# Optimization experiments

Hardware: AMD Instinct MI355X
Metric: run time of the kernel (lower is better)

Reference implementation:

```python
import jax, jax.numpy as jnp
import numpy as np

NSAMPLE = 16   # knn neighbors for cost volume
KCLUST = 8     # cluster size stand-in for custom_cluster_pc1 (min_count=8)
B, N, D = 2, 4096, 64


def _sqdist(src, dst):
    # src [B,N,C], dst [B,M,C] -> [B,N,M]
    d = (jnp.sum(src * src, -1)[:, :, None]
         + jnp.sum(dst * dst, -1)[:, None, :]
         - 2.0 * jnp.einsum('bnc,bmc->bnm', src, dst))
    return jnp.maximum(d, 0.0)


def _knn(k, xyz, new_xyz):
    return jax.lax.top_k(-_sqdist(new_xyz, xyz), k)[1]  # [B,S,k] indices of k smallest


def _group(points, idx):
    # points [B,M,C], idx [B,N,K] -> [B,N,K,C]
    b = jnp.arange(points.shape[0])[:, None, None]
    return points[b, idx]


def _weightnet(x, w1, b1, w2, b2, w3, b3):
    # x [B,N,K,3]; 1x1 conv stack == per-point MLP, relu
    h = jax.nn.relu(jnp.einsum('bnkc,cd->bnkd', x, w1) + b1)
    h = jax.nn.relu(jnp.einsum('bnkc,cd->bnkd', h, w2) + b2)
    return jax.nn.relu(jnp.einsum('bnkc,cd->bnkd', h, w3) + b3)


def _leaky(x):
    return jnp.where(x > 0, x, 0.1 * x)


def _forward(xyz1, xyz2, points1, points2, vel1, vel2, mask1, mask2,
             w_xyz, w_vel, w_points,
             mlp_w1, mlp_b1, mlp_w2, mlp_b2,
             wn1_w1, wn1_b1, wn1_w2, wn1_b2, wn1_w3, wn1_b3,
             wn2_w1, wn2_b1, wn2_w2, wn2_b2, wn2_w3, wn2_b3):
    xyz1t = jnp.transpose(xyz1, (0, 2, 1))      # [B,N1,3]
    xyz2t = jnp.transpose(xyz2, (0, 2, 1))      # [B,N2,3]
    p1t = jnp.transpose(points1, (0, 2, 1))     # [B,N1,D1]
    p2t = jnp.transpose(points2, (0, 2, 1))     # [B,N2,D2]

    # --- custom_cluster_pc1 stand-in: knn clusters of pc1 with its velocities ---
    idx_c = _knn(KCLUST, xyz1t, xyz1t)                     # [B,N,KC]
    cc = _group(xyz1t, idx_c)                              # [B,N,KC,3]
    cv = _group(vel1[..., None], idx_c)[..., 0]            # [B,N,KC]

    u = cc / jnp.linalg.norm(cc, axis=-1, keepdims=True)
    ATA = jnp.einsum('bnki,bnkj->bnij', u, u) + 1e-6 * jnp.eye(3, dtype=u.dtype)
    ATb = jnp.einsum('bnki,bnk->bni', u, cv)
    v_world = jnp.linalg.solve(ATA, ATb[..., None])[..., 0]  # [B,N,3]

    # --- feature-space knn between weighted (xyz, points) concatenations ---
    f1 = jnp.concatenate([w_xyz * xyz1t, w_points * p1t], axis=-1)
    f2 = jnp.concatenate([w_xyz * xyz2t, w_points * p2t], axis=-1)
    knn_idx = _knn(NSAMPLE, f2, f1)                        # [B,N1,K]

    neighbor_xyz = _group(xyz2t, knn_idx)                  # [B,N1,K,3]
    direction_xyz = neighbor_xyz - xyz1t[:, :, None, :]
    g2 = _group(p2t, knn_idx)                              # [B,N1,K,D2]
    g1 = jnp.broadcast_to(p1t[:, :, None, :], g2.shape[:3] + (p1t.shape[-1],))
    new_points = jnp.concatenate([g1, g2, direction_xyz], axis=-1)  # [B,N1,K,D1+D2+3]

    h = _leaky(jnp.einsum('bnkc,cd->bnkd', new_points, mlp_w1) + mlp_b1)
    h = _leaky(jnp.einsum('bnkc,cd->bnkd', h, mlp_w2) + mlp_b2)    # [B,N1,K,128]

    w = _weightnet(direction_xyz, wn1_w1, wn1_b1, wn1_w2, wn1_b2, wn1_w3, wn1_b3)
    point_to_patch = jnp.sum(w * h, axis=2)                # [B,N1,128]

    # --- second grouping in rigid-velocity space ---
    idx2 = _knn(NSAMPLE, v_world, v_world)
    nxyz1 = _group(xyz1t, idx2)
    dir2 = nxyz1 - xyz1t[:, :, None, :]
    w2 = _weightnet(dir2, wn2_w1, wn2_b1, wn2_w2, wn2_b2, wn2_w3, wn2_b3)
    gcost = _group(point_to_patch, idx2)                   # [B,N1,K,128]
    patch_to_patch = jnp.sum(w2 * gcost, axis=2)           # [B,N1,128]

    return jnp.transpose(patch_to_patch, (0, 2, 1)), v_world  # [B,128,N1], [B,N1,3]


def setup_inputs() -> dict:
    key = jax.random.key(0)
    ks = jax.random.split(key, 24)
    s = 0.05
    inp = {
        'xyz1': jax.random.normal(ks[0], (B, 3, N), jnp.float32),
        'xyz2': jax.random.normal(ks[1], (B, 3, N), jnp.float32),
        'points1': jax.random.normal(ks[2], (B, D, N), jnp.float32),
        'points2': jax.random.normal(ks[3], (B, D, N), jnp.float32),
        'vel1': jax.random.normal(ks[4], (B, N), jnp.float32),
        'vel2': jax.random.normal(ks[5], (B, N), jnp.float32),
        'mask1': jnp.ones((B, N), jnp.float32),
        'mask2': jnp.ones((B, N), jnp.float32),
        'w_xyz': jnp.float32(0.4), 'w_vel': jnp.float32(0.2), 'w_points': jnp.float32(0.4),
        'mlp_w1': jax.random.normal(ks[6], (2 * D + 3, 128), jnp.float32) * s,
        'mlp_b1': jnp.zeros((128,), jnp.float32),
        'mlp_w2': jax.random.normal(ks[7], (128, 128), jnp.float32) * s,
        'mlp_b2': jnp.zeros((128,), jnp.float32),
    }
    for tag, base in (('wn1', 8), ('wn2', 14)):
        inp[f'{tag}_w1'] = jax.random.normal(ks[base], (3, 8), jnp.float32) * s
        inp[f'{tag}_b1'] = jnp.zeros((8,), jnp.float32)
        inp[f'{tag}_w2'] = jax.random.normal(ks[base + 1], (8, 8), jnp.float32) * s
        inp[f'{tag}_b2'] = jnp.zeros((8,), jnp.float32)
        inp[f'{tag}_w3'] = jax.random.normal(ks[base + 2], (8, 128), jnp.float32) * s
        inp[f'{tag}_b3'] = jnp.zeros((128,), jnp.float32)
    return inp


def reference(xyz1, xyz2, points1, points2, vel1, vel2, mask1, mask2,
              w_xyz, w_vel, w_points,
              mlp_w1, mlp_b1, mlp_w2, mlp_b2,
              wn1_w1, wn1_b1, wn1_w2, wn1_b2, wn1_w3, wn1_b3,
              wn2_w1, wn2_b1, wn2_w2, wn2_b2, wn2_w3, wn2_b3):
    return _forward(xyz1, xyz2, points1, points2, vel1, vel2, mask1, mask2,
                    w_xyz, w_vel, w_points,
                    mlp_w1, mlp_b1, mlp_w2, mlp_b2,
                    wn1_w1, wn1_b1, wn1_w2, wn1_b2, wn1_w3, wn1_b3,
                    wn2_w1, wn2_b1, wn2_w2, wn2_b2, wn2_w3, wn2_b3)
```

## Files before the change

### kernel.cpp

```cpp
#include <hip/hip_runtime.h>

#define NPTS 4096
#define NQ   8192
#define DD   64
#define KNN  16
#define KC   8
#define NSEG3 32
#define NPSEG 32
#define KB96 96
#define FSTR 104
#define VOFF 1048576

#define ALWAYS_INLINE __attribute__((always_inline)) inline

typedef __attribute__((ext_vector_type(8))) short bf16x8;
typedef __attribute__((ext_vector_type(4))) float f32x4;

__device__ ALWAYS_INLINE float leakyf(float x) { return x > 0.f ? x : 0.1f * x; }

__device__ ALWAYS_INLINE unsigned short bf16rne(float f) {
  unsigned u = __float_as_uint(f);
  u = (u + 0x7FFFu + ((u >> 16) & 1u)) >> 16;
  return (unsigned short)u;
}

__device__ ALWAYS_INLINE float packdt(float d, unsigned tag12) {
  return __uint_as_float((__float_as_uint(d) & 0xFFFFF000u) | tag12);
}

#define TK8_FOREACH(M)  M(0) M(1) M(2) M(3) M(4) M(5) M(6) M(7)
#define TK16_FOREACH(M) M(0) M(1) M(2) M(3) M(4) M(5) M(6) M(7) \
                        M(8) M(9) M(10) M(11) M(12) M(13) M(14) M(15)

#define TK_DECL1(i) float tkd##i = 3.4e38f; int tki##i = 0;
#define TK_STEP1(i) { bool c = vd < tkd##i; float t_ = tkd##i; int u_ = tki##i; \
                      tkd##i = c ? vd : tkd##i; tki##i = c ? vi : tki##i; \
                      vd = c ? t_ : vd; vi = c ? u_ : vi; }
#define TK8_DECL  TK8_FOREACH(TK_DECL1)
#define TK8_INS(dexp, mexp)  { float vd = (dexp); int vi = (mexp); \
                               if (vd < tkd7)  { TK8_FOREACH(TK_STEP1) } }
#define TK8_RESET1(i) tkd##i = 3.4e38f; tki##i = 0;

#define PK_DECL1(i) float pk##i = __uint_as_float(0x7F7FFFFFu);
#define PK_RESET1(i) pk##i = __uint_as_float(0x7F7FFFFFu);
#define PK_STEP1(i) { float lo_ = fminf(pk##i, pv); pv = fmaxf(pk##i, pv); pk##i = lo_; }
#define PK16_DECL    TK16_FOREACH(PK_DECL1)
#define PK16_INS(ve) { float pv = (ve); TK16_FOREACH(PK_STEP1) }
#define PK_STORE1(i) pdq[i] = pk##i;
#define PK16_STORE   TK16_FOREACH(PK_STORE1)

__global__ __launch_bounds__(256) void k_prep(
    const float* __restrict__ xyz1, const float* __restrict__ xyz2,
    const float* __restrict__ pts1, const float* __restrict__ pts2,
    const float* __restrict__ w_xyz_p, const float* __restrict__ w_points_p,
    unsigned short* __restrict__ f1b, unsigned short* __restrict__ f2b,
    float* __restrict__ n1, float* __restrict__ n2a,
    float* __restrict__ p1t, float* __restrict__ p2t,
    float* __restrict__ x1t, float* __restrict__ x2t)
{
  int tgid = blockIdx.x * 256 + threadIdx.x;
  int cloud = tgid >> 13;
  int gid = tgid & (NQ - 1);
  int b = gid >> 12, n = gid & (NPTS - 1);
  float wx = w_xyz_p[0], wp = w_points_p[0];
  const float* xyz = cloud ? xyz2 : xyz1;
  const float* pts = cloud ? pts2 : pts1;
  unsigned short* fb = cloud ? f2b : f1b;
  float* nrm = cloud ? n2a : n1;
  float* pt  = cloud ? p2t : p1t;
  float* xt  = cloud ? x2t : x1t;
  const float* xb = xyz + (size_t)b * 3 * NPTS;
  float x = xb[n], y = xb[NPTS + n], z = xb[2 * NPTS + n];
  float nrm2 = fmaf(z, z, fmaf(y, y, x * x));
  float4 xv; xv.x = x; xv.y = y; xv.z = z; xv.w = nrm2;
  *(float4*)&xt[(size_t)gid * 4] = xv;
  float fx = wx * x, fy = wx * y, fz = wx * z;
  float acc = fmaf(fz, fz, fmaf(fy, fy, fx * fx));
  unsigned short* fr = fb + (size_t)gid * KB96;
  fr[0] = bf16rne(fx); fr[1] = bf16rne(fy); fr[2] = bf16rne(fz);
  const float* pb = pts + (size_t)b * DD * NPTS;
  float* pr = pt + (size_t)gid * DD;
  for (int c = 0; c < DD; ++c) {
    float v = pb[(size_t)c * NPTS + n];
    pr[c] = v;
    float fv = wp * v;
    fr[3 + c] = bf16rne(fv);
    acc = fmaf(fv, fv, acc);
  }
  for (int c = 67; c < KB96; ++c) fr[c] = 0;
  nrm[gid] = acc;
}

__global__ __launch_bounds__(256) void k_knn3(
    const float* __restrict__ x4, float* __restrict__ pd, int* __restrict__ pi)
{
  __shared__ __align__(16) float4 sc[128];
  int seg = blockIdx.y;
  int Q = blockIdx.x * 256 + threadIdx.x;
  int b = Q >> 12;
  float4 q = *(const float4*)&x4[(size_t)Q * 4];
  TK8_DECL
  int gbase = (b << 12) + seg * 128;
  if (threadIdx.x < 128)
    sc[threadIdx.x] = *(const float4*)&x4[(size_t)(gbase + threadIdx.x) * 4];
  __syncthreads();
  int m0 = seg * 128;
#pragma unroll
  for (int j = 0; j < 128; ++j) {
    float4 c = sc[j];
    float dot = fmaf(q.z, c.z, fmaf(q.y, c.y, q.x * c.x));
    float d = fmaxf(q.w + c.w - 2.f * dot, 0.f);
    TK8_INS(d, m0 + j)
  }
  float* pdq = pd + ((size_t)Q * NSEG3 + seg) * 8;
  int* piq = pi + ((size_t)Q * NSEG3 + seg) * 8;
#define ST8(i) pdq[i] = tkd##i; piq[i] = tki##i;
  TK8_FOREACH(ST8)
#undef ST8
}

__global__ __launch_bounds__(256) void k_knnv(
    const float* __restrict__ x4, float* __restrict__ pd)
{
  __shared__ __align__(16) float4 sc[128];
  int seg = blockIdx.y;
  int Q = blockIdx.x * 256 + threadIdx.x;
  int b = Q >> 12;
  float4 q = *(const float4*)&x4[(size_t)Q * 4];
  PK16_DECL
  int gbase = (b << 12) + seg * 128;
  if (threadIdx.x < 128)
    sc[threadIdx.x] = *(const float4*)&x4[(size_t)(gbase + threadIdx.x) * 4];
  __syncthreads();
#pragma unroll
  for (int j = 0; j < 128; ++j) {
    float4 c = sc[j];
    float dot = fmaf(q.z, c.z, fmaf(q.y, c.y, q.x * c.x));
    float d = fmaxf(q.w + c.w - 2.f * dot, 0.f);
    PK16_INS(packdt(d, ((unsigned)j << 5) | (unsigned)seg))
  }
  float* pdq = pd + ((size_t)Q * NPSEG + seg) * 16;
  PK16_STORE
}

__global__ __launch_bounds__(256) void k_rigid(
    const float* __restrict__ pd, const int* __restrict__ pi,
    const float* __restrict__ x4, const float* __restrict__ vel1,
    float* __restrict__ vout, float* __restrict__ v4out)
{
  __shared__ __align__(16) float s_d[64][33];
  __shared__ __align__(16) int   s_i[64][33];
  int tid = threadIdx.x;
  int ql = tid >> 2, part = tid & 3;
  int Q = blockIdx.x * 64 + ql;
  int b = Q >> 12;
  TK8_DECL
  {
    int s0 = part * 8;
    const float* pbase = pd + ((size_t)Q * NSEG3 + s0) * 8;
    const int* ibase = pi + ((size_t)Q * NSEG3 + s0) * 8;
#pragma unroll
    for (int s = 0; s < 8; ++s) {
#pragma unroll
      for (int j = 0; j < 8; ++j) TK8_INS(pbase[s * 8 + j], ibase[s * 8 + j])
    }
  }
#define STP(i) s_d[ql][part * 8 + i] = tkd##i; s_i[ql][part * 8 + i] = tki##i;
  TK8_FOREACH(STP)
#undef STP
  __syncthreads();
  if (part != 0) return;
  TK8_FOREACH(TK8_RESET1)
#pragma unroll
  for (int j = 0; j < 32; ++j) TK8_INS(s_d[ql][j], s_i[ql][j])
  int base = b << 12;
  double a00 = 0, a01 = 0, a02 = 0, a11 = 0, a12 = 0, a22 = 0;
  double r0 = 0, r1 = 0, r2 = 0;
#define RIG_ACC(i) { \
    float4 c = *(const float4*)&x4[(size_t)(base + tki##i) * 4]; \
    float nr = sqrtf(c.w); \
    float ux = c.x / nr, uy = c.y / nr, uz = c.z / nr; \
    float cv = vel1[base + tki##i]; \
    double dx = ux, dy = uy, dz = uz, dvv = cv; \
    a00 += dx * dx; a01 += dx * dy; a02 += dx * dz; \
    a11 += dy * dy; a12 += dy * dz; a22 += dz * dz; \
    r0 += dx * dvv; r1 += dy * dvv; r2 += dz * dvv; }
  TK8_FOREACH(RIG_ACC)
#undef RIG_ACC
  a00 += 1e-6; a11 += 1e-6; a22 += 1e-6;
  double c00 = a11 * a22 - a12 * a12;
  double c01 = a02 * a12 - a01 * a22;
  double c02 = a01 * a12 - a02 * a11;
  double c11 = a00 * a22 - a02 * a02;
  double c12 = a02 * a01 - a00 * a12;
  double c22 = a00 * a11 - a01 * a01;
  double det = a00 * c00 + a01 * c01 + a02 * c02;
  double inv = 1.0 / det;
  float vx = (float)((c00 * r0 + c01 * r1 + c02 * r2) * inv);
  float vy = (float)((c01 * r0 + c11 * r1 + c12 * r2) * inv);
  float vz = (float)((c02 * r0 + c12 * r1 + c22 * r2) * inv);
  vout[(size_t)Q * 3 + 0] = vx;
  vout[(size_t)Q * 3 + 1] = vy;
  vout[(size_t)Q * 3 + 2] = vz;
  float4 v; v.x = vx; v.y = vy; v.z = vz;
  v.w = fmaf(vz, vz, fmaf(vy, vy, vx * vx));
  *(float4*)&v4out[(size_t)Q * 4] = v;
}

__global__ __launch_bounds__(256) void k_knnf_mfma(
    const unsigned short* __restrict__ f1b, const unsigned short* __restrict__ f2b,
    const float* __restrict__ n1, const float* __restrict__ n2a,
    float* __restrict__ pd)
{
  __shared__ __align__(16) unsigned short sf1[16 * FSTR];
  __shared__ __align__(16) unsigned short sf2[2][64 * FSTR];
  __shared__ __align__(16) float sn1[16];
  __shared__ __align__(16) float sn2[2][64];
  __shared__ __align__(16) float sD[64][17];
  int tid = threadIdx.x;
  int w = tid >> 6, lane = tid & 63;
  int i15 = lane & 15, g = lane >> 4, kr0 = g * 8;
  int blockq = blockIdx.x * 16;
  int b = blockq >> 12;
  int seg = blockIdx.y;
  int gbase = (b << 12) + seg * 2048;
  {
    const float4* src = (const float4*)(f1b + (size_t)blockq * KB96);
    if (tid < 192) ((float4*)sf1)[tid + tid / 12] = src[tid];
    if (tid < 16) sn1[tid] = n1[blockq + tid];
  }
  {
    const float4* src = (const float4*)(f2b + (size_t)gbase * KB96);
    int i0 = tid, i1 = tid + 256, i2 = tid + 512;
    ((float4*)sf2[0])[i0 + i0 / 12] = src[i0];
    ((float4*)sf2[0])[i1 + i1 / 12] = src[i1];
    ((float4*)sf2[0])[i2 + i2 / 12] = src[i2];
    if (tid < 64) sn2[0][tid] = n2a[gbase + tid];
  }
  __syncthreads();
  bf16x8 af0 = *(const bf16x8*)&sf1[i15 * FSTR + kr0];
  bf16x8 af1 = *(const bf16x8*)&sf1[i15 * FSTR + 32 + kr0];
  bf16x8 af2 = *(const bf16x8*)&sf1[i15 * FSTR + 64 + kr0];
  float nq0 = sn1[g * 4 + 0], nq1 = sn1[g * 4 + 1];
  float nq2 = sn1[g * 4 + 2], nq3 = sn1[g * 4 + 3];
  PK16_DECL
  int q_tk = tid & 15, p_tk = tid >> 4;
  for (int ch = 0; ch < 32; ++ch) {
    int cur = ch & 1;
    {
      int crow = w * 16 + i15;
      const unsigned short* c_ = &sf2[cur][crow * FSTR + kr0];
      f32x4 acc = {0.f, 0.f, 0.f, 0.f};
      acc = __builtin_amdgcn_mfma_f32_16x16x32_bf16(af0, *(const bf16x8*)&c_[0],  acc, 0, 0, 0);
      acc = __builtin_amdgcn_mfma_f32_16x16x32_bf16(af1, *(const bf16x8*)&c_[32], acc, 0, 0, 0);
      acc = __builtin_amdgcn_mfma_f32_16x16x32_bf16(af2, *(const bf16x8*)&c_[64], acc, 0, 0, 0);
      float nn2 = sn2[cur][crow];
      unsigned tag = (((unsigned)(ch * 4 + (crow & 3))) << 5) |
                     (unsigned)(seg * 16 + (crow >> 2));
      sD[crow][g * 4 + 0] = packdt(fmaxf(nq0 + nn2 - 2.f * acc[0], 0.f), tag);
      sD[crow][g * 4 + 1] = packdt(fmaxf(nq1 + nn2 - 2.f * acc[1], 0.f), tag);
      sD[crow][g * 4 + 2] = packdt(fmaxf(nq2 + nn2 - 2.f * acc[2], 0.f), tag);
      sD[crow][g * 4 + 3] = packdt(fmaxf(nq3 + nn2 - 2.f * acc[3], 0.f), tag);
    }
    __syncthreads();
    if (ch + 1 < 32) {
      const float4* src = (const float4*)(f2b + (size_t)(gbase + (ch + 1) * 64) * KB96);
      int i0 = tid, i1 = tid + 256, i2 = tid + 512;
      ((float4*)sf2[cur ^ 1])[i0 + i0 / 12] = src[i0];
      ((float4*)sf2[cur ^ 1])[i1 + i1 / 12] = src[i1];
      ((float4*)sf2[cur ^ 1])[i2 + i2 / 12] = src[i2];
      if (tid < 64) sn2[cur ^ 1][tid] = n2a[gbase + (ch + 1) * 64 + tid];
    }
#pragma unroll
    for (int j = 0; j < 4; ++j)
      PK16_INS(sD[p_tk * 4 + j][q_tk])
    __syncthreads();
  }
  int pseg = seg * 16 + p_tk;
  float* pdq = pd + ((size_t)(blockq + q_tk) * NPSEG + pseg) * 16;
  PK16_STORE
}

template<int MODE>
__global__ __launch_bounds__(256) void k_mergepk(
    const float* __restrict__ pd, int* __restrict__ oidx)
{
  __shared__ __align__(16) float s_k[64][65];
  int tid = threadIdx.x;
  int ql = tid >> 2, part = tid & 3;
  int Q = blockIdx.x * 64 + ql;
  PK16_DECL
  {
    const float* pbase = pd + ((size_t)Q * NPSEG + part * 8) * 16;
#pragma unroll
    for (int s = 0; s < 8; ++s) {
      for (int j = 0; j < 16; ++j) {
        float v = pbase[s * 16 + j];
        if (!(v < pk15)) break;
        PK16_INS(v)
      }
    }
  }
#define STK(i) s_k[ql][part * 16 + i] = pk##i;
  TK16_FOREACH(STK)
#undef STK
  __syncthreads();
  if (part != 0) return;
  TK16_FOREACH(PK_RESET1)
#pragma unroll
  for (int p = 0; p < 4; ++p) {
    for (int j = 0; j < 16; ++j) {
      float v = s_k[ql][p * 16 + j];
      if (!(v < pk15)) break;
      PK16_INS(v)
    }
  }
#define DEC(i) { unsigned u = __float_as_uint(pk##i); int m_; \
    unsigned ps = u & 31u, lo = (u >> 5) & 127u; \
    if (MODE == 0) m_ = (int)(((ps >> 4) << 11) + ((lo >> 2) << 6) + ((ps & 15u) << 2) + (lo & 3u)); \
    else m_ = (int)((ps << 7) + lo); \
    oidx[(size_t)Q * KNN + i] = m_; }
  TK16_FOREACH(DEC)
#undef DEC
}

#define PPB 8
__device__ ALWAYS_INLINE bf16x8 load_wfrag(const float* __restrict__ Wg,
                                           int kbase, int col, int kmax) {
  bf16x8 r;
#pragma unroll
  for (int j = 0; j < 8; ++j) {
    int k = kbase + j;
    float f = (k < kmax) ? Wg[(size_t)k * 128 + col] : 0.f;
    r[j] = (short)bf16rne(f);
  }
  return r;
}

__global__ __launch_bounds__(512) void k_mlp_mfma(
    const float* __restrict__ p1t, const float* __restrict__ p2t,
    const float* __restrict__ x1t, const float* __restrict__ x2t,
    const int* __restrict__ kidx,
    const float* __restrict__ W1, const float* __restrict__ B1v,
    const float* __restrict__ W2, const float* __restrict__ B2v,
    const float* __restrict__ wnw1, const float* __restrict__ wnb1,
    const float* __restrict__ wnw2, const float* __restrict__ wnb2,
    const float* __restrict__ wnw3, const float* __restrict__ wnb3,
    float* __restrict__ ptp)
{
  __shared__ __align__(16) unsigned short sA1[16 * 168];
  __shared__ __align__(16) unsigned short sH1[16 * 136];
  __shared__ __align__(16) float s_wv[16 * 128];
  __shared__ __align__(16) float s_c1[24];
  __shared__ __align__(16) float s_cb1[8];
  __shared__ __align__(16) float s_c2[64];
  __shared__ __align__(16) float s_cb2[8];
  __shared__ __align__(16) float s_w3[1024];
  __shared__ __align__(16) float s_b3[128];
  int tid = threadIdx.x;
  int w = tid >> 6, lane = tid & 63;
  int col = (w << 4) + (lane & 15);
  int kr0 = (lane >> 4) * 8;
  if (tid < 24) s_c1[tid] = wnw1[tid];
  else if (tid < 32) s_cb1[tid - 24] = wnb1[tid - 24];
  else if (tid < 96) s_c2[tid - 32] = wnw2[tid - 32];
  else if (tid < 104) s_cb2[tid - 96] = wnb2[tid - 96];
  if (tid >= 128 && tid < 256) s_b3[tid - 128] = wnb3[tid - 128];
  for (int i = tid; i < 1024; i += 512) s_w3[i] = wnw3[i];
  bf16x8 w1f0 = load_wfrag(W1, 0 + kr0, col, 131);
  bf16x8 w1f1 = load_wfrag(W1, 32 + kr0, col, 131);
  bf16x8 w1f2 = load_wfrag(W1, 64 + kr0, col, 131);
  bf16x8 w1f3 = load_wfrag(W1, 96 + kr0, col, 131);
  bf16x8 w1f4 = load_wfrag(W1, 128 + kr0, col, 131);
  bf16x8 w2f0 = load_wfrag(W2, 0 + kr0, col, 128);
  bf16x8 w2f1 = load_wfrag(W2, 32 + kr0, col, 128);
  bf16x8 w2f2 = load_wfrag(W2, 64 + kr0, col, 128);
  bf16x8 w2f3 = load_wfrag(W2, 96 + kr0, col, 128);
  float b1c = B1v[col], b2c = B2v[col];
  int blk0 = blockIdx.x * PPB;
  int base = (blk0 >> 12) << 12;
  int r_st = tid >> 5, t_st = tid & 31;

  for (int p = 0; p < PPB; ++p) {
    int gid = blk0 + p;
    __syncthreads();
    {
      int m = kidx[(size_t)gid * 16 + r_st];
      int grow = base + m;
      float4 cx1 = *(const float4*)&x1t[(size_t)gid * 4];
      float4 cx2 = *(const float4*)&x2t[(size_t)grow * 4];
      unsigned short* row = &sA1[r_st * 168];
      row[t_st]      = bf16rne(p1t[(size_t)gid * 64 + t_st]);
      row[t_st + 32] = bf16rne(p1t[(size_t)gid * 64 + t_st + 32]);
      row[t_st + 64] = bf16rne(p2t[(size_t)grow * 64 + t_st]);
      row[t_st + 96] = bf16rne(p2t[(size_t)grow * 64 + t_st + 32]);
      float dx = cx2.x - cx1.x, dy = cx2.y - cx1.y, dz = cx2.z - cx1.z;
      float dv_ = (t_st == 0) ? dx : (t_st == 1) ? dy : (t_st == 2) ? dz : 0.f;
      row[t_st + 128] = bf16rne(dv_);
      float h1w0 = fmaxf(fmaf(dz, s_c1[16], fmaf(dy, s_c1[8],  fmaf(dx, s_c1[0], s_cb1[0]))), 0.f);
      float h1w1 = fmaxf(fmaf(dz, s_c1[17], fmaf(dy, s_c1[9],  fmaf(dx, s_c1[1], s_cb1[1]))), 0.f);
      float h1w2 = fmaxf(fmaf(dz, s_c1[18], fmaf(dy, s_c1[10], fmaf(dx, s_c1[2], s_cb1[2]))), 0.f);
      float h1w3 = fmaxf(fmaf(dz, s_c1[19], fmaf(dy, s_c1[11], fmaf(dx, s_c1[3], s_cb1[3]))), 0.f);
      float h1w4 = fmaxf(fmaf(dz, s_c1[20], fmaf(dy, s_c1[12], fmaf(dx, s_c1[4], s_cb1[4]))), 0.f);
      float h1w5 = fmaxf(fmaf(dz, s_c1[21], fmaf(dy, s_c1[13], fmaf(dx, s_c1[5], s_cb1[5]))), 0.f);
      float h1w6 = fmaxf(fmaf(dz, s_c1[22], fmaf(dy, s_c1[14], fmaf(dx, s_c1[6], s_cb1[6]))), 0.f);
      float h1w7 = fmaxf(fmaf(dz, s_c1[23], fmaf(dy, s_c1[15], fmaf(dx, s_c1[7], s_cb1[7]))), 0.f);
#define H2W(j) float h2w##j; { float a_ = s_cb2[j]; \
      a_ = fmaf(h1w0, s_c2[0 * 8 + j], a_); a_ = fmaf(h1w1, s_c2[1 * 8 + j], a_); \
      a_ = fmaf(h1w2, s_c2[2 * 8 + j], a_); a_ = fmaf(h1w3, s_c2[3 * 8 + j], a_); \
      a_ = fmaf(h1w4, s_c2[4 * 8 + j], a_); a_ = fmaf(h1w5, s_c2[5 * 8 + j], a_); \
      a_ = fmaf(h1w6, s_c2[6 * 8 + j], a_); a_ = fmaf(h1w7, s_c2[7 * 8 + j], a_); \
      h2w##j = fmaxf(a_, 0.f); }
      H2W(0) H2W(1) H2W(2) H2W(3) H2W(4) H2W(5) H2W(6) H2W(7)
#undef H2W
      int c4 = t_st * 4;
      float4 wv = *(const float4*)&s_b3[c4];
#define WV(j) { float4 w3 = *(const float4*)&s_w3[j * 128 + c4]; \
      wv.x = fmaf(h2w##j, w3.x, wv.x); wv.y = fmaf(h2w##j, w3.y, wv.y); \
      wv.z = fmaf(h2w##j, w3.z, wv.z); wv.w = fmaf(h2w##j, w3.w, wv.w); }
      WV(0) WV(1) WV(2) WV(3) WV(4) WV(5) WV(6) WV(7)
#undef WV
      wv.x = fmaxf(wv.x, 0.f); wv.y = fmaxf(wv.y, 0.f);
      wv.z = fmaxf(wv.z, 0.f); wv.w = fmaxf(wv.w, 0.f);
      *(float4*)&s_wv[r_st * 128 + c4] = wv;
    }
    __syncthreads();
    {
      int ab = (lane & 15) * 168 + kr0;
      f32x4 acc = {0.f, 0.f, 0.f, 0.f};
      acc = __builtin_amdgcn_mfma_f32_16x16x32_bf16(*(const bf16x8*)&sA1[ab],       w1f0, acc, 0, 0, 0);
      acc = __builtin_amdgcn_mfma_f32_16x16x32_bf16(*(const bf16x8*)&sA1[ab + 32],  w1f1, acc, 0, 0, 0);
      acc = __builtin_amdgcn_mfma_f32_16x16x32_bf16(*(const bf16x8*)&sA1[ab + 64],  w1f2, acc, 0, 0, 0);
      acc = __builtin_amdgcn_mfma_f32_16x16x32_bf16(*(const bf16x8*)&sA1[ab + 96],  w1f3, acc, 0, 0, 0);
      acc = __builtin_amdgcn_mfma_f32_16x16x32_bf16(*(const bf16x8*)&sA1[ab + 128], w1f4, acc, 0, 0, 0);
      int rw0 = (lane >> 4) * 4;
#pragma unroll
      for (int r = 0; r < 4; ++r)
        sH1[(rw0 + r) * 136 + col] = bf16rne(leakyf(acc[r] + b1c));
    }
    __syncthreads();
    {
      int ab = (lane & 15) * 136 + kr0;
      f32x4 acc = {0.f, 0.f, 0.f, 0.f};
      acc = __builtin_amdgcn_mfma_f32_16x16x32_bf16(*(const bf16x8*)&sH1[ab],      w2f0, acc, 0, 0, 0);
      acc = __builtin_amdgcn_mfma_f32_16x16x32_bf16(*(const bf16x8*)&sH1[ab + 32], w2f1, acc, 0, 0, 0);
      acc = __builtin_amdgcn_mfma_f32_16x16x32_bf16(*(const bf16x8*)&sH1[ab + 64], w2f2, acc, 0, 0, 0);
      acc = __builtin_amdgcn_mfma_f32_16x16x32_bf16(*(const bf16x8*)&sH1[ab + 96], w2f3, acc, 0, 0, 0);
      int rw0 = (lane >> 4) * 4;
      float v = 0.f;
#pragma unroll
      for (int r = 0; r < 4; ++r)
        v = fmaf(s_wv[(rw0 + r) * 128 + col], leakyf(acc[r] + b2c), v);
      v += __shfl_xor(v, 16);
      v += __shfl_xor(v, 32);
      if (lane < 16) ptp[(size_t)gid * 128 + col] = v;
    }
  }
}

__global__ __launch_bounds__(256) void k_final(
    const float* __restrict__ x1t, const int* __restrict__ idx2,
    const float* __restrict__ ptp,
    const float* __restrict__ wnw1, const float* __restrict__ wnb1,
    const float* __restrict__ wnw2, const float* __restrict__ wnb2,
    const float* __restrict__ wnw3, const float* __restrict__ wnb3,
    float* __restrict__ out0)
{
  __shared__ __align__(16) float s_gc[16][128];
  __shared__ __align__(16) float s_wn[16][8];
  __shared__ __align__(16) float s_red[2][128];
  int gid = blockIdx.x, b = gid >> 12, n = gid & (NPTS - 1);
  int tid = threadIdx.x;
  if (tid < 16) {
    int m = idx2[(size_t)gid * 16 + tid];
    float4 c2 = *(const float4*)&x1t[(size_t)((b << 12) + m) * 4];
    float4 c1 = *(const float4*)&x1t[(size_t)gid * 4];
    float dx = c2.x - c1.x, dy = c2.y - c1.y, dz = c2.z - c1.z;
    float h1w[8];
#pragma unroll
    for (int j = 0; j < 8; ++j)
      h1w[j] = fmaxf(fmaf(dz, wnw1[16 + j], fmaf(dy, wnw1[8 + j], fmaf(dx, wnw1[j], wnb1[j]))), 0.f);
#pragma unroll
    for (int j = 0; j < 8; ++j) {
      float a = wnb2[j];
#pragma unroll
      for (int qq = 0; qq < 8; ++qq) a = fmaf(h1w[qq], wnw2[qq * 8 + j], a);
      s_wn[tid][j] = fmaxf(a, 0.f);
    }
  }
  int k2 = tid >> 4, i2 = tid & 15;
  int mg = idx2[(size_t)gid * 16 + k2];
  const float* src = &ptp[(size_t)((b << 12) + mg) * 128 + i2 * 8];
  *(float4*)&s_gc[k2][i2 * 8] = *(const float4*)&src[0];
  *(float4*)&s_gc[k2][i2 * 8 + 4] = *(const float4*)&src[4];
  __syncthreads();
  int ch = tid & 127, kg2 = tid >> 7;
  float r = 0.f;
#pragma unroll
  for (int jj = 0; jj < 8; ++jj) {
    int k = kg2 * 8 + jj;
    float4 wa = *(const float4*)&s_wn[k][0];
    float4 wb = *(const float4*)&s_wn[k][4];
    float wv = wnb3[ch];
    wv = fmaf(wa.x, wnw3[ch], wv);
    wv = fmaf(wa.y, wnw3[128 + ch], wv);
    wv = fmaf(wa.z, wnw3[256 + ch], wv);
    wv = fmaf(wa.w, wnw3[384 + ch], wv);
    wv = fmaf(wb.x, wnw3[512 + ch], wv);
    wv = fmaf(wb.y, wnw3[640 + ch], wv);
    wv = fmaf(wb.z, wnw3[768 + ch], wv);
    wv = fmaf(wb.w, wnw3[896 + ch], wv);
    wv = fmaxf(wv, 0.f);
    r = fmaf(wv, s_gc[k][ch], r);
  }
  s_red[kg2][ch] = r;
  __syncthreads();
  if (tid < 128)
    out0[(size_t)(b * 128 + tid) * NPTS + n] = s_red[0][tid] + s_red[1][tid];
}

extern "C" void kernel_launch(void* const* d_in, const int* in_sizes, int n_in,
                              void* d_out, int out_size, void* d_ws, size_t ws_size,
                              hipStream_t stream) {
  (void)in_sizes; (void)n_in; (void)out_size; (void)ws_size;
  const float* xyz1   = (const float*)d_in[0];
  const float* xyz2   = (const float*)d_in[1];
  const float* pts1   = (const float*)d_in[2];
  const float* pts2   = (const float*)d_in[3];
  const float* vel1   = (const float*)d_in[4];
  const float* w_xyz  = (const float*)d_in[8];
  const float* w_pts  = (const float*)d_in[10];
  const float* mlp_w1 = (const float*)d_in[11];
  const float* mlp_b1 = (const float*)d_in[12];
  const float* mlp_w2 = (const float*)d_in[13];
  const float* mlp_b2 = (const float*)d_in[14];
  const float* wn1_w1 = (const float*)d_in[15];
  const float* wn1_b1 = (const float*)d_in[16];
  const float* wn1_w2 = (const float*)d_in[17];
  const float* wn1_b2 = (const float*)d_in[18];
  const float* wn1_w3 = (const float*)d_in[19];
  const float* wn1_b3 = (const float*)d_in[20];
  const float* wn2_w1 = (const float*)d_in[21];
  const float* wn2_b1 = (const float*)d_in[22];
  const float* wn2_w2 = (const float*)d_in[23];
  const float* wn2_b2 = (const float*)d_in[24];
  const float* wn2_w3 = (const float*)d_in[25];
  const float* wn2_b3 = (const float*)d_in[26];

  char* ws = (char*)d_ws;
  size_t off = 0;
  float* pd   = (float*)(ws + off); off += (size_t)NQ * NPSEG * 16 * 4;
  int*   pi   = (int*)(ws + off);   off += (size_t)NQ * NSEG3 * 8 * 4;
  unsigned short* f1b = (unsigned short*)(ws + off); off += (size_t)NQ * KB96 * 2;
  unsigned short* f2b = (unsigned short*)(ws + off); off += (size_t)NQ * KB96 * 2;
  float* n1   = (float*)(ws + off); off += (size_t)NQ * 4;
  float* n2a  = (float*)(ws + off); off += (size_t)NQ * 4;
  float* p1t  = (float*)(ws + off); off += (size_t)NQ * DD * 4;
  float* p2t  = (float*)(ws + off); off += (size_t)NQ * DD * 4;
  float* x1t  = (float*)(ws + off); off += (size_t)NQ * 4 * 4;
  float* x2t  = (float*)(ws + off); off += (size_t)NQ * 4 * 4;
  int*   kidx = (int*)(ws + off);   off += (size_t)NQ * KNN * 4;
  float* ptp  = (float*)(ws + off); off += (size_t)NQ * 128 * 4;
  int*   idx2 = (int*)(ws + off);   off += (size_t)NQ * KNN * 4;
  float* v4   = (float*)(ws + off); off += (size_t)NQ * 4 * 4;

  float* out0 = (float*)d_out;
  float* outv = (float*)d_out + VOFF;

  k_prep<<<64, 256, 0, stream>>>(xyz1, xyz2, pts1, pts2, w_xyz, w_pts,
                                 f1b, f2b, n1, n2a, p1t, p2t, x1t, x2t);
  k_knn3<<<dim3(32, NSEG3), 256, 0, stream>>>(x1t, pd, pi);
  k_rigid<<<128, 256, 0, stream>>>(pd, pi, x1t, vel1, outv, v4);
  k_knnf_mfma<<<dim3(NQ / 16, 2), 256, 0, stream>>>(f1b, f2b, n1, n2a, pd);
  k_mergepk<0><<<128, 256, 0, stream>>>(pd, kidx);
  k_mlp_mfma<<<NQ / PPB, 512, 0, stream>>>(p1t, p2t, x1t, x2t, kidx,
                                           mlp_w1, mlp_b1, mlp_w2, mlp_b2,
                                           wn1_w1, wn1_b1, wn1_w2, wn1_b2,
                                           wn1_w3, wn1_b3, ptp);
  k_knnv<<<dim3(32, 32), 256, 0, stream>>>(v4, pd);
  k_mergepk<1><<<128, 256, 0, stream>>>(pd, idx2);
  k_final<<<NQ, 256, 0, stream>>>(x1t, idx2, ptp,
                                  wn2_w1, wn2_b1, wn2_w2, wn2_b2, wn2_w3, wn2_b3, out0);
}
```

Measured before the change: 347.4 us.

## Fuse top-k partial merges into consumer kernels and widen prep parallelism

Removes the two standalone k_mergepk launches and performs the segment-wise top-16 merge inside k_mlp_mfma and k_final, keeping the decoded neighbour indices in shared memory. This drops two kernel launches and the round trip of index arrays through global memory. k_prep is also split so that four threads handle each point's channels, with a shared-memory reduction for the norm, giving four times as many blocks. The cost is that the merge now runs on only a few threads per block (32 and then 8 in the MLP kernel, 4 and then 1 in k_final), adding serial latency to those kernels before their main work starts.

```diff
diff --git a/kernel.cpp b/kernel.cpp
--- a/kernel.cpp
+++ b/kernel.cpp
@@ -58,9 +58,11 @@
     float* __restrict__ p1t, float* __restrict__ p2t,
     float* __restrict__ x1t, float* __restrict__ x2t)
 {
-  int tgid = blockIdx.x * 256 + threadIdx.x;
-  int cloud = tgid >> 13;
-  int gid = tgid & (NQ - 1);
+  __shared__ float s_acc[64][5];
+  int tid = threadIdx.x;
+  int nl = tid & 63, part = tid >> 6;
+  int cloud = blockIdx.x >> 7;
+  int gid = ((blockIdx.x & 127) << 6) + nl;
   int b = gid >> 12, n = gid & (NPTS - 1);
   float wx = w_xyz_p[0], wp = w_points_p[0];
   const float* xyz = cloud ? xyz2 : xyz1;
@@ -69,26 +71,35 @@
   float* nrm = cloud ? n2a : n1;
   float* pt  = cloud ? p2t : p1t;
   float* xt  = cloud ? x2t : x1t;
-  const float* xb = xyz + (size_t)b * 3 * NPTS;
-  float x = xb[n], y = xb[NPTS + n], z = xb[2 * NPTS + n];
-  float nrm2 = fmaf(z, z, fmaf(y, y, x * x));
-  float4 xv; xv.x = x; xv.y = y; xv.z = z; xv.w = nrm2;
-  *(float4*)&xt[(size_t)gid * 4] = xv;
-  float fx = wx * x, fy = wx * y, fz = wx * z;
-  float acc = fmaf(fz, fz, fmaf(fy, fy, fx * fx));
-  unsigned short* fr = fb + (size_t)gid * KB96;
-  fr[0] = bf16rne(fx); fr[1] = bf16rne(fy); fr[2] = bf16rne(fz);
   const float* pb = pts + (size_t)b * DD * NPTS;
   float* pr = pt + (size_t)gid * DD;
-  for (int c = 0; c < DD; ++c) {
-    float v = pb[(size_t)c * NPTS + n];
-    pr[c] = v;
+  unsigned short* fr = fb + (size_t)gid * KB96;
+  int c0 = part * 16;
+  float acc = 0.f;
+#pragma unroll 4
+  for (int j = 0; j < 16; ++j) {
+    float v = pb[(size_t)(c0 + j) * NPTS + n];
+    pr[c0 + j] = v;
     float fv = wp * v;
-    fr[3 + c] = bf16rne(fv);
+    fr[3 + c0 + j] = bf16rne(fv);
     acc = fmaf(fv, fv, acc);
   }
-  for (int c = 67; c < KB96; ++c) fr[c] = 0;
-  nrm[gid] = acc;
+  s_acc[nl][part] = acc;
+  if (part == 1) { for (int c = 67; c < 82; ++c) fr[c] = 0; }
+  else if (part == 2) { for (int c = 82; c < KB96; ++c) fr[c] = 0; }
+  __syncthreads();
+  if (part == 0) {
+    const float* xb = xyz + (size_t)b * 3 * NPTS;
+    float x = xb[n], y = xb[NPTS + n], z = xb[2 * NPTS + n];
+    float nrm2 = fmaf(z, z, fmaf(y, y, x * x));
+    float4 xv; xv.x = x; xv.y = y; xv.z = z; xv.w = nrm2;
+    *(float4*)&xt[(size_t)gid * 4] = xv;
+    float fx = wx * x, fy = wx * y, fz = wx * z;
+    fr[0] = bf16rne(fx); fr[1] = bf16rne(fy); fr[2] = bf16rne(fz);
+    float a = fmaf(fz, fz, fmaf(fy, fy, fx * fx));
+    a += s_acc[nl][0] + s_acc[nl][1] + s_acc[nl][2] + s_acc[nl][3];
+    nrm[gid] = a;
+  }
 }
 
 __global__ __launch_bounds__(256) void k_knn3(
@@ -281,49 +292,6 @@
   PK16_STORE
 }
 
-template<int MODE>
-__global__ __launch_bounds__(256) void k_mergepk(
-    const float* __restrict__ pd, int* __restrict__ oidx)
-{
-  __shared__ __align__(16) float s_k[64][65];
-  int tid = threadIdx.x;
-  int ql = tid >> 2, part = tid & 3;
-  int Q = blockIdx.x * 64 + ql;
-  PK16_DECL
-  {
-    const float* pbase = pd + ((size_t)Q * NPSEG + part * 8) * 16;
-#pragma unroll
-    for (int s = 0; s < 8; ++s) {
-      for (int j = 0; j < 16; ++j) {
-        float v = pbase[s * 16 + j];
-        if (!(v < pk15)) break;
-        PK16_INS(v)
-      }
-    }
-  }
-#define STK(i) s_k[ql][part * 16 + i] = pk##i;
-  TK16_FOREACH(STK)
-#undef STK
-  __syncthreads();
-  if (part != 0) return;
-  TK16_FOREACH(PK_RESET1)
-#pragma unroll
-  for (int p = 0; p < 4; ++p) {
-    for (int j = 0; j < 16; ++j) {
-      float v = s_k[ql][p * 16 + j];
-      if (!(v < pk15)) break;
-      PK16_INS(v)
-    }
-  }
-#define DEC(i) { unsigned u = __float_as_uint(pk##i); int m_; \
-    unsigned ps = u & 31u, lo = (u >> 5) & 127u; \
-    if (MODE == 0) m_ = (int)(((ps >> 4) << 11) + ((lo >> 2) << 6) + ((ps & 15u) << 2) + (lo & 3u)); \
-    else m_ = (int)((ps << 7) + lo); \
-    oidx[(size_t)Q * KNN + i] = m_; }
-  TK16_FOREACH(DEC)
-#undef DEC
-}
-
 #define PPB 8
 __device__ ALWAYS_INLINE bf16x8 load_wfrag(const float* __restrict__ Wg,
                                            int kbase, int col, int kmax) {
@@ -340,7 +308,7 @@
 __global__ __launch_bounds__(512) void k_mlp_mfma(
     const float* __restrict__ p1t, const float* __restrict__ p2t,
     const float* __restrict__ x1t, const float* __restrict__ x2t,
-    const int* __restrict__ kidx,
+    const float* __restrict__ pd,
     const float* __restrict__ W1, const float* __restrict__ B1v,
     const float* __restrict__ W2, const float* __restrict__ B2v,
     const float* __restrict__ wnw1, const float* __restrict__ wnb1,
@@ -357,16 +325,36 @@
   __shared__ __align__(16) float s_cb2[8];
   __shared__ __align__(16) float s_w3[1024];
   __shared__ __align__(16) float s_b3[128];
+  __shared__ __align__(16) float s_mk[8][68];
+  __shared__ int s_kidx[8][16];
   int tid = threadIdx.x;
   int w = tid >> 6, lane = tid & 63;
   int col = (w << 4) + (lane & 15);
   int kr0 = (lane >> 4) * 8;
+  int blk0 = blockIdx.x * PPB;
+  int base = (blk0 >> 12) << 12;
   if (tid < 24) s_c1[tid] = wnw1[tid];
   else if (tid < 32) s_cb1[tid - 24] = wnb1[tid - 24];
   else if (tid < 96) s_c2[tid - 32] = wnw2[tid - 32];
   else if (tid < 104) s_cb2[tid - 96] = wnb2[tid - 96];
   if (tid >= 128 && tid < 256) s_b3[tid - 128] = wnb3[tid - 128];
   for (int i = tid; i < 1024; i += 512) s_w3[i] = wnw3[i];
+  if (tid < 32) {
+    int qm = tid >> 2, pm = tid & 3;
+    PK16_DECL
+    const float* pbase = pd + ((size_t)(blk0 + qm) * NPSEG + pm * 8) * 16;
+#pragma unroll
+    for (int s = 0; s < 8; ++s) {
+      for (int j = 0; j < 16; ++j) {
+        float v = pbase[s * 16 + j];
+        if (!(v < pk15)) break;
+        PK16_INS(v)
+      }
+    }
+#define STK(i) s_mk[qm][pm * 16 + i] = pk##i;
+    TK16_FOREACH(STK)
+#undef STK
+  }
   bf16x8 w1f0 = load_wfrag(W1, 0 + kr0, col, 131);
   bf16x8 w1f1 = load_wfrag(W1, 32 + kr0, col, 131);
   bf16x8 w1f2 = load_wfrag(W1, 64 + kr0, col, 131);
@@ -377,15 +365,30 @@
   bf16x8 w2f2 = load_wfrag(W2, 64 + kr0, col, 128);
   bf16x8 w2f3 = load_wfrag(W2, 96 + kr0, col, 128);
   float b1c = B1v[col], b2c = B2v[col];
-  int blk0 = blockIdx.x * PPB;
-  int base = (blk0 >> 12) << 12;
+  __syncthreads();
+  if (tid < 8) {
+    PK16_DECL
+#pragma unroll
+    for (int pm = 0; pm < 4; ++pm) {
+      for (int j = 0; j < 16; ++j) {
+        float v = s_mk[tid][pm * 16 + j];
+        if (!(v < pk15)) break;
+        PK16_INS(v)
+      }
+    }
+#define DEC(i) { unsigned u = __float_as_uint(pk##i); \
+    unsigned ps = u & 31u, lo = (u >> 5) & 127u; \
+    s_kidx[tid][i] = (int)(((ps >> 4) << 11) + ((lo >> 2) << 6) + ((ps & 15u) << 2) + (lo & 3u)); }
+    TK16_FOREACH(DEC)
+#undef DEC
+  }
   int r_st = tid >> 5, t_st = tid & 31;
 
   for (int p = 0; p < PPB; ++p) {
     int gid = blk0 + p;
     __syncthreads();
     {
-      int m = kidx[(size_t)gid * 16 + r_st];
+      int m = s_kidx[p][r_st];
       int grow = base + m;
       float4 cx1 = *(const float4*)&x1t[(size_t)gid * 4];
       float4 cx2 = *(const float4*)&x2t[(size_t)grow * 4];
@@ -459,7 +462,7 @@
 }
 
 __global__ __launch_bounds__(256) void k_final(
-    const float* __restrict__ x1t, const int* __restrict__ idx2,
+    const float* __restrict__ x1t, const float* __restrict__ pd,
     const float* __restrict__ ptp,
     const float* __restrict__ wnw1, const float* __restrict__ wnb1,
     const float* __restrict__ wnw2, const float* __restrict__ wnb2,
@@ -469,10 +472,45 @@
   __shared__ __align__(16) float s_gc[16][128];
   __shared__ __align__(16) float s_wn[16][8];
   __shared__ __align__(16) float s_red[2][128];
+  __shared__ __align__(16) float s_mk[4][17];
+  __shared__ int s_idx[16];
   int gid = blockIdx.x, b = gid >> 12, n = gid & (NPTS - 1);
   int tid = threadIdx.x;
+  if (tid < 4) {
+    PK16_DECL
+    const float* pbase = pd + ((size_t)gid * NPSEG + tid * 8) * 16;
+#pragma unroll
+    for (int s = 0; s < 8; ++s) {
+      for (int j = 0; j < 16; ++j) {
+        float v = pbase[s * 16 + j];
+        if (!(v < pk15)) break;
+        PK16_INS(v)
+      }
+    }
+#define STK(i) s_mk[tid][i] = pk##i;
+    TK16_FOREACH(STK)
+#undef STK
+  }
+  __syncthreads();
+  if (tid == 0) {
+    PK16_DECL
+#pragma unroll
+    for (int pm = 0; pm < 4; ++pm) {
+      for (int j = 0; j < 16; ++j) {
+        float v = s_mk[pm][j];
+        if (!(v < pk15)) break;
+        PK16_INS(v)
+      }
+    }
+#define DEC(i) { unsigned u = __float_as_uint(pk##i); \
+    unsigned ps = u & 31u, lo = (u >> 5) & 127u; \
+    s_idx[i] = (int)((ps << 7) + lo); }
+    TK16_FOREACH(DEC)
+#undef DEC
+  }
+  __syncthreads();
   if (tid < 16) {
-    int m = idx2[(size_t)gid * 16 + tid];
+    int m = s_idx[tid];
     float4 c2 = *(const float4*)&x1t[(size_t)((b << 12) + m) * 4];
     float4 c1 = *(const float4*)&x1t[(size_t)gid * 4];
     float dx = c2.x - c1.x, dy = c2.y - c1.y, dz = c2.z - c1.z;
@@ -489,7 +527,7 @@
     }
   }
   int k2 = tid >> 4, i2 = tid & 15;
-  int mg = idx2[(size_t)gid * 16 + k2];
+  int mg = s_idx[k2];
   const float* src = &ptp[(size_t)((b << 12) + mg) * 128 + i2 * 8];
   *(float4*)&s_gc[k2][i2 * 8] = *(const float4*)&src[0];
   *(float4*)&s_gc[k2][i2 * 8 + 4] = *(const float4*)&src[4];
@@ -559,26 +597,22 @@
   float* p2t  = (float*)(ws + off); off += (size_t)NQ * DD * 4;
   float* x1t  = (float*)(ws + off); off += (size_t)NQ * 4 * 4;
   float* x2t  = (float*)(ws + off); off += (size_t)NQ * 4 * 4;
-  int*   kidx = (int*)(ws + off);   off += (size_t)NQ * KNN * 4;
   float* ptp  = (float*)(ws + off); off += (size_t)NQ * 128 * 4;
-  int*   idx2 = (int*)(ws + off);   off += (size_t)NQ * KNN * 4;
   float* v4   = (float*)(ws + off); off += (size_t)NQ * 4 * 4;
 
   float* out0 = (float*)d_out;
   float* outv = (float*)d_out + VOFF;
 
-  k_prep<<<64, 256, 0, stream>>>(xyz1, xyz2, pts1, pts2, w_xyz, w_pts,
-                                 f1b, f2b, n1, n2a, p1t, p2t, x1t, x2t);
+  k_prep<<<256, 256, 0, stream>>>(xyz1, xyz2, pts1, pts2, w_xyz, w_pts,
+                                  f1b, f2b, n1, n2a, p1t, p2t, x1t, x2t);
   k_knn3<<<dim3(32, NSEG3), 256, 0, stream>>>(x1t, pd, pi);
   k_rigid<<<128, 256, 0, stream>>>(pd, pi, x1t, vel1, outv, v4);
   k_knnf_mfma<<<dim3(NQ / 16, 2), 256, 0, stream>>>(f1b, f2b, n1, n2a, pd);
-  k_mergepk<0><<<128, 256, 0, stream>>>(pd, kidx);
-  k_mlp_mfma<<<NQ / PPB, 512, 0, stream>>>(p1t, p2t, x1t, x2t, kidx,
+  k_mlp_mfma<<<NQ / PPB, 512, 0, stream>>>(p1t, p2t, x1t, x2t, pd,
                                            mlp_w1, mlp_b1, mlp_w2, mlp_b2,
                                            wn1_w1, wn1_b1, wn1_w2, wn1_b2,
                                            wn1_w3, wn1_b3, ptp);
   k_knnv<<<dim3(32, 32), 256, 0, stream>>>(v4, pd);
-  k_mergepk<1><<<128, 256, 0, stream>>>(pd, idx2);
-  k_final<<<NQ, 256, 0, stream>>>(x1t, idx2, ptp,
+  k_final<<<NQ, 256, 0, stream>>>(x1t, pd, ptp,
                                   wn2_w1, wn2_b1, wn2_w2, wn2_b2, wn2_w3, wn2_b3, out0);
 }
```

Result: slower. 525.8 us (+51.3%).
